# Kernel tuning notes

Hardware: AMD Instinct MI355X
Metric: run time of the kernel (lower is better)

The kernel has to match this reference:

```python
import jax, jax.numpy as jnp
import numpy as np
import math

B, T, D, H = 8, 1024, 512, 8
HD = D // H  # head_dim = 64


def setup_inputs() -> dict:
    key = jax.random.key(0)
    ks = jax.random.split(key, 16)
    s = 1.0 / math.sqrt(D)
    inp = {
        "x": jax.random.normal(ks[0], (B, T, D), jnp.float32),
        "pos": jax.random.normal(ks[1], (B, T, D), jnp.float32),
        "mask": jnp.ones((B, T, T), dtype=bool),
        "Wq": jax.random.normal(ks[2], (D, D), jnp.float32) * s,
        "bq": jax.random.normal(ks[3], (D,), jnp.float32) * s,
        "Wk": jax.random.normal(ks[4], (D, D), jnp.float32) * s,
        "bk": jax.random.normal(ks[5], (D,), jnp.float32) * s,
        "Wv": jax.random.normal(ks[6], (D, D), jnp.float32) * s,
        "bv": jax.random.normal(ks[7], (D,), jnp.float32) * s,
        "Wp": jax.random.normal(ks[8], (D, D), jnp.float32) * s,
        "Wo": jax.random.normal(ks[9], (D, D), jnp.float32) * s,
        "bo": jax.random.normal(ks[10], (D,), jnp.float32) * s,
        "pos_bias_u": jax.random.normal(ks[11], (H, HD), jnp.float32) * 0.02,
        "pos_bias_v": jax.random.normal(ks[12], (H, HD), jnp.float32) * 0.02,
    }
    return inp


def _shape(t):
    # [B, T, D] -> [B, H, T, HD]
    b, n, _ = t.shape
    return t.reshape(b, n, H, HD).transpose(0, 2, 1, 3)


def _relative_shift(s):
    # s: [B, H, Tq, Tk]
    b, h, tq, tk = s.shape
    s = jnp.pad(s, ((0, 0), (0, 0), (0, 0), (1, 0)))  # zero pad on left of last dim
    s = s.reshape(b, h, tk + 1, tq)[:, :, 1:, :].reshape(b, h, tq, tk)
    return s


def reference(x, pos, mask, Wq, bq, Wk, bk, Wv, bv, Wp, Wo, bo, pos_bias_u, pos_bias_v):
    q = _shape(x @ Wq + bq)          # [B,H,T,HD]
    k = _shape(x @ Wk + bk)
    v = _shape(x @ Wv + bv)
    p = _shape(pos @ Wp)             # pos_proj has no bias

    q_u = q + pos_bias_u[None, :, None, :]
    q_v = q + pos_bias_v[None, :, None, :]

    content = jnp.einsum("bhqd,bhkd->bhqk", q_u, k)
    position = jnp.einsum("bhqd,bhkd->bhqk", q_v, p)
    position = _relative_shift(position)[..., : content.shape[-1]]

    scores = (content + position) / math.sqrt(HD)
    scores = jnp.where(mask[:, None, :, :], scores, -1e9)
    attn = jax.nn.softmax(scores, axis=-1)

    ctx = jnp.einsum("bhqk,bhkd->bhqd", attn, v)
    ctx = ctx.transpose(0, 2, 1, 3).reshape(x.shape[0], x.shape[1], D)
    return ctx @ Wo + bo
```

## Files before the change

kernel.cpp:

```cpp
#include <hip/hip_runtime.h>
#include <cstdint>
#include <cstddef>

typedef unsigned short u16;
typedef unsigned int u32;
typedef __attribute__((ext_vector_type(8))) short bf16x8;
typedef __attribute__((ext_vector_type(4))) float f32x4;

#define LOG2E 1.4426950408889634f

__device__ __forceinline__ u16 f2bf(float f) {
  u32 u = __builtin_bit_cast(u32, f);
  u += 0x7fffu + ((u >> 16) & 1u);
  return (u16)(u >> 16);
}
__device__ __forceinline__ float bf2f(u16 h) {
  u32 u = ((u32)h) << 16;
  return __builtin_bit_cast(float, u);
}
__device__ __forceinline__ void g2l16(const void* g, void* l) {
  __builtin_amdgcn_global_load_lds((const __attribute__((address_space(1))) void*)g,
                                   (__attribute__((address_space(3))) void*)l, 16, 0, 0);
}

__global__ void cvt_bf16(const float* __restrict__ in, u16* __restrict__ out, int n) {
  int i = (blockIdx.x * blockDim.x + threadIdx.x) * 4;
  if (i >= n) return;
  float4 v = *(const float4*)(in + i);
  ushort4 o;
  o.x = f2bf(v.x); o.y = f2bf(v.y); o.z = f2bf(v.z); o.w = f2bf(v.w);
  *(ushort4*)(out + i) = o;
}

__global__ void transp_bf16(const float* __restrict__ W, u16* __restrict__ Wt) {
  __shared__ float t[64][65];
  const int n0 = blockIdx.x * 64, k0 = blockIdx.y * 64;
  const int tid = threadIdx.x;
  const int tx = tid & 63, ty = tid >> 6;
#pragma unroll
  for (int i = 0; i < 16; ++i) {
    int kl = ty + i * 4;
    t[kl][tx] = W[(size_t)(k0 + kl) * 512 + n0 + tx];
  }
  __syncthreads();
#pragma unroll
  for (int i = 0; i < 16; ++i) {
    int nl = ty + i * 4;
    Wt[(size_t)(n0 + nl) * 512 + k0 + tx] = f2bf(t[tx][nl]);
  }
}

__global__ __launch_bounds__(256, 2) void proj_gemm(
    const u16* __restrict__ xb, const u16* __restrict__ posb, const u16* __restrict__ Wt,
    const float* __restrict__ bq, const float* __restrict__ bk, const float* __restrict__ bv,
    const float* __restrict__ pbu, const float* __restrict__ pbv,
    u16* __restrict__ qu, u16* __restrict__ qv, u16* __restrict__ kb,
    u16* __restrict__ vT, u16* __restrict__ pb) {
  __shared__ __align__(16) u16 As[128 * 64];
  __shared__ __align__(16) u16 Bs[128 * 64];
  const int m0 = blockIdx.x * 128;
  const int nt = blockIdx.y;
  const int n0 = nt * 128;
  const int sec = nt >> 2;
  const u16* A = (sec == 3) ? posb : xb;
  const int tid = threadIdx.x;
  const int wid = tid >> 6, lane = tid & 63;
  const int wr = (wid >> 1) * 64, wc = (wid & 1) * 64;
  const int l15 = lane & 15, l4 = lane >> 4;
  f32x4 acc[4][4] = {};
  for (int k0 = 0; k0 < 512; k0 += 64) {
    __syncthreads();
#pragma unroll
    for (int i = 0; i < 4; ++i) {
      int s = tid + i * 256;
      int row = s >> 3, sl = s & 7, ssl = sl ^ (row & 7);
      g2l16(A + (size_t)(m0 + row) * 512 + k0 + ssl * 8, &As[s * 8]);
      g2l16(Wt + (size_t)(n0 + row) * 512 + k0 + ssl * 8, &Bs[s * 8]);
    }
    __syncthreads();
    bf16x8 af[4][2], bfr[4][2];
#pragma unroll
    for (int mi = 0; mi < 4; ++mi)
#pragma unroll
      for (int kk = 0; kk < 2; ++kk) {
        int row = wr + mi * 16 + l15;
        int slot = (kk * 4 + l4) ^ (row & 7);
        af[mi][kk] = *(const bf16x8*)&As[row * 64 + slot * 8];
      }
#pragma unroll
    for (int ni = 0; ni < 4; ++ni)
#pragma unroll
      for (int kk = 0; kk < 2; ++kk) {
        int row = wc + ni * 16 + l15;
        int slot = (kk * 4 + l4) ^ (row & 7);
        bfr[ni][kk] = *(const bf16x8*)&Bs[row * 64 + slot * 8];
      }
#pragma unroll
    for (int mi = 0; mi < 4; ++mi)
#pragma unroll
      for (int ni = 0; ni < 4; ++ni)
#pragma unroll
        for (int kk = 0; kk < 2; ++kk)
          acc[mi][ni] = __builtin_amdgcn_mfma_f32_16x16x32_bf16(af[mi][kk], bfr[ni][kk], acc[mi][ni], 0, 0, 0);
  }
#pragma unroll
  for (int mi = 0; mi < 4; ++mi)
#pragma unroll
    for (int ni = 0; ni < 4; ++ni) {
      int ng = n0 + wc + ni * 16 + l15;
      int cs = ng & 511;
      int h = cs >> 6, d = cs & 63;
      float bias = (sec == 0) ? bq[cs] : (sec == 1) ? bk[cs] : (sec == 2) ? bv[cs] : 0.f;
#pragma unroll
      for (int r = 0; r < 4; ++r) {
        int mg = m0 + wr + mi * 16 + l4 * 4 + r;
        int b = mg >> 10, t = mg & 1023;
        int bh = b * 8 + h;
        float val = acc[mi][ni][r] + bias;
        if (sec == 0) {
          size_t o = (size_t)bh * 65536 + (size_t)t * 64 + d;
          qu[o] = f2bf(val + pbu[cs]);
          qv[o] = f2bf(val + pbv[cs]);
        } else if (sec == 1) {
          kb[(size_t)bh * 65536 + (size_t)t * 64 + d] = f2bf(val);
        } else if (sec == 2) {
          vT[(size_t)bh * 65536 + (size_t)d * 1024 + t] = f2bf(val);
        } else {
          pb[(size_t)bh * 65536 + (size_t)t * 64 + d] = f2bf(val);
        }
      }
    }
}

__global__ __launch_bounds__(256, 2) void pos_shift_gemm(
    const u16* __restrict__ qv, const u16* __restrict__ pb, u16* __restrict__ spos) {
  __shared__ __align__(16) u16 As[128 * 64];
  __shared__ __align__(16) u16 Bs[128 * 64];
  const int bh = blockIdx.z;
  const int i0 = blockIdx.y * 128, j0 = blockIdx.x * 128;
  const u16* A = qv + (size_t)bh * 65536;
  const u16* B = pb + (size_t)bh * 65536;
  u16* S = spos + (size_t)bh * 1048576;
  const int tid = threadIdx.x;
  const int wid = tid >> 6, lane = tid & 63;
  const int wr = (wid >> 1) * 64, wc = (wid & 1) * 64;
  const int l15 = lane & 15, l4 = lane >> 4;
#pragma unroll
  for (int i = 0; i < 4; ++i) {
    int s = tid + i * 256;
    int row = s >> 3, sl = s & 7, ssl = sl ^ (row & 7);
    g2l16(A + (size_t)(i0 + row) * 64 + ssl * 8, &As[s * 8]);
    g2l16(B + (size_t)(j0 + row) * 64 + ssl * 8, &Bs[s * 8]);
  }
  __syncthreads();
  f32x4 acc[4][4] = {};
  bf16x8 af[4][2], bfr[4][2];
#pragma unroll
  for (int mi = 0; mi < 4; ++mi)
#pragma unroll
    for (int kk = 0; kk < 2; ++kk) {
      int row = wr + mi * 16 + l15;
      int slot = (kk * 4 + l4) ^ (row & 7);
      af[mi][kk] = *(const bf16x8*)&As[row * 64 + slot * 8];
    }
#pragma unroll
  for (int ni = 0; ni < 4; ++ni)
#pragma unroll
    for (int kk = 0; kk < 2; ++kk) {
      int row = wc + ni * 16 + l15;
      int slot = (kk * 4 + l4) ^ (row & 7);
      bfr[ni][kk] = *(const bf16x8*)&Bs[row * 64 + slot * 8];
    }
#pragma unroll
  for (int mi = 0; mi < 4; ++mi)
#pragma unroll
    for (int ni = 0; ni < 4; ++ni)
#pragma unroll
      for (int kk = 0; kk < 2; ++kk)
        acc[mi][ni] = __builtin_amdgcn_mfma_f32_16x16x32_bf16(af[mi][kk], bfr[ni][kk], acc[mi][ni], 0, 0, 0);
#pragma unroll
  for (int mi = 0; mi < 4; ++mi)
#pragma unroll
    for (int ni = 0; ni < 4; ++ni) {
      int j = j0 + wc + ni * 16 + l15;
#pragma unroll
      for (int r = 0; r < 4; ++r) {
        int i_ = i0 + wr + mi * 16 + l4 * 4 + r;
        float val = acc[mi][ni][r] * 0.125f;
        if (j >= 1023 - i_) {
          S[(size_t)i_ * 1024 + (size_t)(i_ + j - 1023)] = f2bf(val);
        } else if (i_ > 0) {
          S[(size_t)(i_ - 1) * 1024 + (size_t)(i_ + j + 1)] = f2bf(val);
        }
      }
    }
}

__global__ __launch_bounds__(256, 2) void flash_attn(
    const u16* __restrict__ qu, const u16* __restrict__ kb,
    const u16* __restrict__ vT, const u16* __restrict__ spos,
    u16* __restrict__ ctx) {
  __shared__ __align__(16) u16 Ks[64 * 64];
  __shared__ __align__(16) u16 Vs[64 * 64];
  __shared__ __align__(16) u16 Ss[64 * 64];
  __shared__ __align__(16) u16 Ps[4 * 16 * 64];
  const int q0 = blockIdx.x * 64;
  const int bh = blockIdx.y;
  const int b = bh >> 3, h = bh & 7;
  const int tid = threadIdx.x;
  const int w = tid >> 6, lane = tid & 63;
  const int l15 = lane & 15, l4 = lane >> 4;
  const u16* Q = qu + (size_t)bh * 65536;
  const u16* K = kb + (size_t)bh * 65536;
  const u16* V = vT + (size_t)bh * 65536;
  const u16* SP = spos + (size_t)bh * 1048576;
  bf16x8 aq[2];
#pragma unroll
  for (int kk = 0; kk < 2; ++kk)
    aq[kk] = *(const bf16x8*)(Q + (size_t)(q0 + w * 16 + l15) * 64 + kk * 32 + l4 * 8);
  f32x4 oacc[4] = {};
  float m_r[4], l_r[4];
#pragma unroll
  for (int r = 0; r < 4; ++r) { m_r[r] = -1e30f; l_r[r] = 0.f; }
  for (int kt = 0; kt < 16; ++kt) {
    const int k0 = kt * 64;
    __syncthreads();
#pragma unroll
    for (int i = 0; i < 2; ++i) {
      int s = tid + i * 256;
      int row = s >> 3, sl = s & 7, ssl = sl ^ (row & 7);
      g2l16(K + (size_t)(k0 + row) * 64 + ssl * 8, &Ks[s * 8]);
      g2l16(V + (size_t)row * 1024 + k0 + ssl * 8, &Vs[s * 8]);
      g2l16(SP + (size_t)(q0 + row) * 1024 + k0 + ssl * 8, &Ss[s * 8]);
    }
    __syncthreads();
    f32x4 sacc[4];
#pragma unroll
    for (int ni = 0; ni < 4; ++ni) {
      f32x4 a = {};
#pragma unroll
      for (int kk = 0; kk < 2; ++kk) {
        int key = ni * 16 + l15;
        int slot = (kk * 4 + l4) ^ (key & 7);
        bf16x8 bfr = *(const bf16x8*)&Ks[key * 64 + slot * 8];
        a = __builtin_amdgcn_mfma_f32_16x16x32_bf16(aq[kk], bfr, a, 0, 0, 0);
      }
      sacc[ni] = a;
    }
    float pvv[4][4], pmax[4];
#pragma unroll
    for (int r = 0; r < 4; ++r) pmax[r] = -1e30f;
#pragma unroll
    for (int ni = 0; ni < 4; ++ni)
#pragma unroll
      for (int r = 0; r < 4; ++r) {
        int srow = w * 16 + l4 * 4 + r;
        int scol = ni * 16 + l15;
        int slot = (scol >> 3) ^ (srow & 7);
        float sv = bf2f(Ss[srow * 64 + slot * 8 + (scol & 7)]);
        if (k0 + scol == q0 + srow + 1) sv = 0.f;
        float s_val = sacc[ni][r] * 0.125f + sv;
        pvv[ni][r] = s_val;
        pmax[r] = fmaxf(pmax[r], s_val);
      }
#pragma unroll
    for (int r = 0; r < 4; ++r)
#pragma unroll
      for (int off = 1; off < 16; off <<= 1)
        pmax[r] = fmaxf(pmax[r], __shfl_xor(pmax[r], off));
    float scl[4], rsum[4];
#pragma unroll
    for (int r = 0; r < 4; ++r) {
      float mn = fmaxf(m_r[r], pmax[r]);
      scl[r] = exp2f((m_r[r] - mn) * LOG2E);
      m_r[r] = mn;
      rsum[r] = 0.f;
    }
#pragma unroll
    for (int ni = 0; ni < 4; ++ni)
#pragma unroll
      for (int r = 0; r < 4; ++r) {
        float p = exp2f((pvv[ni][r] - m_r[r]) * LOG2E);
        pvv[ni][r] = p;
        rsum[r] += p;
      }
#pragma unroll
    for (int r = 0; r < 4; ++r) {
#pragma unroll
      for (int off = 1; off < 16; off <<= 1)
        rsum[r] += __shfl_xor(rsum[r], off);
      l_r[r] = l_r[r] * scl[r] + rsum[r];
    }
#pragma unroll
    for (int ni = 0; ni < 4; ++ni) {
      f32x4 o = oacc[ni];
      o[0] *= scl[0]; o[1] *= scl[1]; o[2] *= scl[2]; o[3] *= scl[3];
      oacc[ni] = o;
    }
#pragma unroll
    for (int ni = 0; ni < 4; ++ni)
#pragma unroll
      for (int r = 0; r < 4; ++r) {
        int prow = l4 * 4 + r;
        int col = ni * 16 + l15;
        int slot = (col >> 3) ^ (prow & 7);
        Ps[w * 1024 + prow * 64 + slot * 8 + (col & 7)] = f2bf(pvv[ni][r]);
      }
    bf16x8 pa[2];
#pragma unroll
    for (int kk = 0; kk < 2; ++kk) {
      int slot = (kk * 4 + l4) ^ (l15 & 7);
      pa[kk] = *(const bf16x8*)&Ps[w * 1024 + l15 * 64 + slot * 8];
    }
#pragma unroll
    for (int ni = 0; ni < 4; ++ni)
#pragma unroll
      for (int kk = 0; kk < 2; ++kk) {
        int drow = ni * 16 + l15;
        int slot = (kk * 4 + l4) ^ (drow & 7);
        bf16x8 vfr = *(const bf16x8*)&Vs[drow * 64 + slot * 8];
        oacc[ni] = __builtin_amdgcn_mfma_f32_16x16x32_bf16(pa[kk], vfr, oacc[ni], 0, 0, 0);
      }
  }
#pragma unroll
  for (int ni = 0; ni < 4; ++ni)
#pragma unroll
    for (int r = 0; r < 4; ++r) {
      int t = q0 + w * 16 + l4 * 4 + r;
      int d = ni * 16 + l15;
      ctx[((size_t)(b * 1024 + t)) * 512 + h * 64 + d] = f2bf(oacc[ni][r] / l_r[r]);
    }
}

__global__ __launch_bounds__(256, 2) void out_gemm(
    const u16* __restrict__ ctx, const u16* __restrict__ Wot,
    const float* __restrict__ bo, float* __restrict__ out) {
  __shared__ __align__(16) u16 As[128 * 64];
  __shared__ __align__(16) u16 Bs[128 * 64];
  const int m0 = blockIdx.x * 128;
  const int n0 = blockIdx.y * 128;
  const int tid = threadIdx.x;
  const int wid = tid >> 6, lane = tid & 63;
  const int wr = (wid >> 1) * 64, wc = (wid & 1) * 64;
  const int l15 = lane & 15, l4 = lane >> 4;
  f32x4 acc[4][4] = {};
  for (int k0 = 0; k0 < 512; k0 += 64) {
    __syncthreads();
#pragma unroll
    for (int i = 0; i < 4; ++i) {
      int s = tid + i * 256;
      int row = s >> 3, sl = s & 7, ssl = sl ^ (row & 7);
      g2l16(ctx + (size_t)(m0 + row) * 512 + k0 + ssl * 8, &As[s * 8]);
      g2l16(Wot + (size_t)(n0 + row) * 512 + k0 + ssl * 8, &Bs[s * 8]);
    }
    __syncthreads();
    bf16x8 af[4][2], bfr[4][2];
#pragma unroll
    for (int mi = 0; mi < 4; ++mi)
#pragma unroll
      for (int kk = 0; kk < 2; ++kk) {
        int row = wr + mi * 16 + l15;
        int slot = (kk * 4 + l4) ^ (row & 7);
        af[mi][kk] = *(const bf16x8*)&As[row * 64 + slot * 8];
      }
#pragma unroll
    for (int ni = 0; ni < 4; ++ni)
#pragma unroll
      for (int kk = 0; kk < 2; ++kk) {
        int row = wc + ni * 16 + l15;
        int slot = (kk * 4 + l4) ^ (row & 7);
        bfr[ni][kk] = *(const bf16x8*)&Bs[row * 64 + slot * 8];
      }
#pragma unroll
    for (int mi = 0; mi < 4; ++mi)
#pragma unroll
      for (int ni = 0; ni < 4; ++ni)
#pragma unroll
        for (int kk = 0; kk < 2; ++kk)
          acc[mi][ni] = __builtin_amdgcn_mfma_f32_16x16x32_bf16(af[mi][kk], bfr[ni][kk], acc[mi][ni], 0, 0, 0);
  }
#pragma unroll
  for (int mi = 0; mi < 4; ++mi)
#pragma unroll
    for (int ni = 0; ni < 4; ++ni) {
      int ng = n0 + wc + ni * 16 + l15;
      float bias = bo[ng];
#pragma unroll
      for (int r = 0; r < 4; ++r) {
        int mg = m0 + wr + mi * 16 + l4 * 4 + r;
        out[(size_t)mg * 512 + ng] = acc[mi][ni][r] + bias;
      }
    }
}

extern "C" void kernel_launch(void* const* d_in, const int* in_sizes, int n_in,
                              void* d_out, int out_size, void* d_ws, size_t ws_size,
                              hipStream_t stream) {
  const float* x   = (const float*)d_in[0];
  const float* pos = (const float*)d_in[1];
  const float* Wq  = (const float*)d_in[3];
  const float* bq  = (const float*)d_in[4];
  const float* Wk  = (const float*)d_in[5];
  const float* bk  = (const float*)d_in[6];
  const float* Wv  = (const float*)d_in[7];
  const float* bv  = (const float*)d_in[8];
  const float* Wp  = (const float*)d_in[9];
  const float* Wo  = (const float*)d_in[10];
  const float* bo  = (const float*)d_in[11];
  const float* pbu = (const float*)d_in[12];
  const float* pbv = (const float*)d_in[13];
  float* out = (float*)d_out;
  char* ws = (char*)d_ws;
  const size_t MB = 1024 * 1024;
  u16* x_bf   = (u16*)(ws);
  u16* pos_bf = (u16*)(ws + 8 * MB);
  u16* Wcat   = (u16*)(ws + 16 * MB);
  u16* Wot    = (u16*)(ws + 18 * MB);
  u16* qu     = (u16*)(ws + 19 * MB);
  u16* qv     = (u16*)(ws + 27 * MB);
  u16* kbuf   = (u16*)(ws + 35 * MB);
  u16* vbuf   = (u16*)(ws + 43 * MB);
  u16* pbuf   = (u16*)(ws + 51 * MB);
  u16* spos   = (u16*)(ws + 59 * MB);
  u16* ctxb   = (u16*)(ws + 187 * MB);

  cvt_bf16<<<4096, 256, 0, stream>>>(x, x_bf, 8192 * 512);
  cvt_bf16<<<4096, 256, 0, stream>>>(pos, pos_bf, 8192 * 512);
  dim3 tg(8, 8);
  transp_bf16<<<tg, 256, 0, stream>>>(Wq, Wcat);
  transp_bf16<<<tg, 256, 0, stream>>>(Wk, Wcat + 512 * 512);
  transp_bf16<<<tg, 256, 0, stream>>>(Wv, Wcat + 2 * 512 * 512);
  transp_bf16<<<tg, 256, 0, stream>>>(Wp, Wcat + 3 * 512 * 512);
  transp_bf16<<<tg, 256, 0, stream>>>(Wo, Wot);
  proj_gemm<<<dim3(64, 16), 256, 0, stream>>>(x_bf, pos_bf, Wcat, bq, bk, bv, pbu, pbv,
                                              qu, qv, kbuf, vbuf, pbuf);
  pos_shift_gemm<<<dim3(8, 8, 64), 256, 0, stream>>>(qv, pbuf, spos);
  flash_attn<<<dim3(16, 64), 256, 0, stream>>>(qu, kbuf, vbuf, spos, ctxb);
  out_gemm<<<dim3(64, 4), 256, 0, stream>>>(ctxb, Wot, bo, out);
}
```

Measured before the change: 326.9 us.

## Fuse relative-shift position scores into flash attention, drop materialized spos

Removes the separate pos_shift_gemm kernel that wrote a full B*H*T*T bf16 shifted position score tensor, and computes the position scores inside flash_attn per tile along diagonals (Q_v times a shifted range of P rows, plus one extra row for the wrap-around). K and V fragments are now read directly from global memory instead of being staged in LDS, and occupancy is raised to 3 blocks. This avoids roughly 128MB of write and read traffic, at the cost of extra MFMA work per tile (a 64x128 diagonal band plus a redundant wave-0 pass) and uncoalesced global fragment loads.

```diff
diff --git a/kernel.cpp b/kernel.cpp
--- a/kernel.cpp
+++ b/kernel.cpp
@@ -132,77 +132,11 @@
     }
 }
 
-__global__ __launch_bounds__(256, 2) void pos_shift_gemm(
-    const u16* __restrict__ qv, const u16* __restrict__ pb, u16* __restrict__ spos) {
-  __shared__ __align__(16) u16 As[128 * 64];
-  __shared__ __align__(16) u16 Bs[128 * 64];
-  const int bh = blockIdx.z;
-  const int i0 = blockIdx.y * 128, j0 = blockIdx.x * 128;
-  const u16* A = qv + (size_t)bh * 65536;
-  const u16* B = pb + (size_t)bh * 65536;
-  u16* S = spos + (size_t)bh * 1048576;
-  const int tid = threadIdx.x;
-  const int wid = tid >> 6, lane = tid & 63;
-  const int wr = (wid >> 1) * 64, wc = (wid & 1) * 64;
-  const int l15 = lane & 15, l4 = lane >> 4;
-#pragma unroll
-  for (int i = 0; i < 4; ++i) {
-    int s = tid + i * 256;
-    int row = s >> 3, sl = s & 7, ssl = sl ^ (row & 7);
-    g2l16(A + (size_t)(i0 + row) * 64 + ssl * 8, &As[s * 8]);
-    g2l16(B + (size_t)(j0 + row) * 64 + ssl * 8, &Bs[s * 8]);
-  }
-  __syncthreads();
-  f32x4 acc[4][4] = {};
-  bf16x8 af[4][2], bfr[4][2];
-#pragma unroll
-  for (int mi = 0; mi < 4; ++mi)
-#pragma unroll
-    for (int kk = 0; kk < 2; ++kk) {
-      int row = wr + mi * 16 + l15;
-      int slot = (kk * 4 + l4) ^ (row & 7);
-      af[mi][kk] = *(const bf16x8*)&As[row * 64 + slot * 8];
-    }
-#pragma unroll
-  for (int ni = 0; ni < 4; ++ni)
-#pragma unroll
-    for (int kk = 0; kk < 2; ++kk) {
-      int row = wc + ni * 16 + l15;
-      int slot = (kk * 4 + l4) ^ (row & 7);
-      bfr[ni][kk] = *(const bf16x8*)&Bs[row * 64 + slot * 8];
-    }
-#pragma unroll
-  for (int mi = 0; mi < 4; ++mi)
-#pragma unroll
-    for (int ni = 0; ni < 4; ++ni)
-#pragma unroll
-      for (int kk = 0; kk < 2; ++kk)
-        acc[mi][ni] = __builtin_amdgcn_mfma_f32_16x16x32_bf16(af[mi][kk], bfr[ni][kk], acc[mi][ni], 0, 0, 0);
-#pragma unroll
-  for (int mi = 0; mi < 4; ++mi)
-#pragma unroll
-    for (int ni = 0; ni < 4; ++ni) {
-      int j = j0 + wc + ni * 16 + l15;
-#pragma unroll
-      for (int r = 0; r < 4; ++r) {
-        int i_ = i0 + wr + mi * 16 + l4 * 4 + r;
-        float val = acc[mi][ni][r] * 0.125f;
-        if (j >= 1023 - i_) {
-          S[(size_t)i_ * 1024 + (size_t)(i_ + j - 1023)] = f2bf(val);
-        } else if (i_ > 0) {
-          S[(size_t)(i_ - 1) * 1024 + (size_t)(i_ + j + 1)] = f2bf(val);
-        }
-      }
-    }
-}
-
-__global__ __launch_bounds__(256, 2) void flash_attn(
-    const u16* __restrict__ qu, const u16* __restrict__ kb,
-    const u16* __restrict__ vT, const u16* __restrict__ spos,
-    u16* __restrict__ ctx) {
-  __shared__ __align__(16) u16 Ks[64 * 64];
-  __shared__ __align__(16) u16 Vs[64 * 64];
-  __shared__ __align__(16) u16 Ss[64 * 64];
+__global__ __launch_bounds__(256, 3) void flash_attn(
+    const u16* __restrict__ qu, const u16* __restrict__ qvg,
+    const u16* __restrict__ kb, const u16* __restrict__ vT,
+    const u16* __restrict__ pbuf, u16* __restrict__ ctx) {
+  __shared__ __align__(16) u16 Sqd[65 * 128];
   __shared__ __align__(16) u16 Ps[4 * 16 * 64];
   const int q0 = blockIdx.x * 64;
   const int bh = blockIdx.y;
@@ -211,27 +145,70 @@
   const int w = tid >> 6, lane = tid & 63;
   const int l15 = lane & 15, l4 = lane >> 4;
   const u16* Q = qu + (size_t)bh * 65536;
+  const u16* QV = qvg + (size_t)bh * 65536;
   const u16* K = kb + (size_t)bh * 65536;
   const u16* V = vT + (size_t)bh * 65536;
-  const u16* SP = spos + (size_t)bh * 1048576;
-  bf16x8 aq[2];
-#pragma unroll
-  for (int kk = 0; kk < 2; ++kk)
-    aq[kk] = *(const bf16x8*)(Q + (size_t)(q0 + w * 16 + l15) * 64 + kk * 32 + l4 * 8);
+  const u16* P = pbuf + (size_t)bh * 65536;
+  bf16x8 aq[2], aqv[2], aqv2[2];
+#pragma unroll
+  for (int kk = 0; kk < 2; ++kk) {
+    aq[kk]  = *(const bf16x8*)(Q  + (size_t)(q0 + w * 16 + l15) * 64 + kk * 32 + l4 * 8);
+    aqv[kk] = *(const bf16x8*)(QV + (size_t)(q0 + w * 16 + l15) * 64 + kk * 32 + l4 * 8);
+  }
+  {
+    int r2 = min(q0 + 64 + l15, 1023);
+#pragma unroll
+    for (int kk = 0; kk < 2; ++kk)
+      aqv2[kk] = *(const bf16x8*)(QV + (size_t)r2 * 64 + kk * 32 + l4 * 8);
+  }
   f32x4 oacc[4] = {};
   float m_r[4], l_r[4];
 #pragma unroll
   for (int r = 0; r < 4; ++r) { m_r[r] = -1e30f; l_r[r] = 0.f; }
   for (int kt = 0; kt < 16; ++kt) {
     const int k0 = kt * 64;
-    __syncthreads();
-#pragma unroll
-    for (int i = 0; i < 2; ++i) {
-      int s = tid + i * 256;
-      int row = s >> 3, sl = s & 7, ssl = sl ^ (row & 7);
-      g2l16(K + (size_t)(k0 + row) * 64 + ssl * 8, &Ks[s * 8]);
-      g2l16(V + (size_t)row * 1024 + k0 + ssl * 8, &Vs[s * 8]);
-      g2l16(SP + (size_t)(q0 + row) * 1024 + k0 + ssl * 8, &Ss[s * 8]);
+    const int dbase = k0 - q0 - 63;
+    __syncthreads();
+#pragma unroll
+    for (int half = 0; half < 2; ++half) {
+      f32x4 pacc[4] = {};
+#pragma unroll
+      for (int ni = 0; ni < 4; ++ni)
+#pragma unroll
+        for (int kk = 0; kk < 2; ++kk) {
+          int n = half * 64 + ni * 16 + l15;
+          int d = dbase + n;
+          int jp = (d <= 0) ? (1023 + d) : (d - 2);
+          jp = min(max(jp, 0), 1023);
+          bf16x8 bp = *(const bf16x8*)(P + (size_t)jp * 64 + kk * 32 + l4 * 8);
+          pacc[ni] = __builtin_amdgcn_mfma_f32_16x16x32_bf16(aqv[kk], bp, pacc[ni], 0, 0, 0);
+        }
+#pragma unroll
+      for (int ni = 0; ni < 4; ++ni)
+#pragma unroll
+        for (int r = 0; r < 4; ++r)
+          Sqd[(w * 16 + l4 * 4 + r) * 128 + half * 64 + ni * 16 + l15] = f2bf(pacc[ni][r] * 0.125f);
+    }
+    if (w == 0) {
+#pragma unroll
+      for (int half = 0; half < 2; ++half) {
+        f32x4 pacc[4] = {};
+#pragma unroll
+        for (int ni = 0; ni < 4; ++ni)
+#pragma unroll
+          for (int kk = 0; kk < 2; ++kk) {
+            int n = half * 64 + ni * 16 + l15;
+            int d = dbase + n;
+            int jp = (d <= 0) ? (1023 + d) : (d - 2);
+            jp = min(max(jp, 0), 1023);
+            bf16x8 bp = *(const bf16x8*)(P + (size_t)jp * 64 + kk * 32 + l4 * 8);
+            pacc[ni] = __builtin_amdgcn_mfma_f32_16x16x32_bf16(aqv2[kk], bp, pacc[ni], 0, 0, 0);
+          }
+        if (l4 == 0)
+#pragma unroll
+          for (int ni = 0; ni < 4; ++ni)
+            Sqd[64 * 128 + half * 64 + ni * 16 + l15] = f2bf(pacc[ni][0] * 0.125f);
+      }
     }
     __syncthreads();
     f32x4 sacc[4];
@@ -240,10 +217,8 @@
       f32x4 a = {};
 #pragma unroll
       for (int kk = 0; kk < 2; ++kk) {
-        int key = ni * 16 + l15;
-        int slot = (kk * 4 + l4) ^ (key & 7);
-        bf16x8 bfr = *(const bf16x8*)&Ks[key * 64 + slot * 8];
-        a = __builtin_amdgcn_mfma_f32_16x16x32_bf16(aq[kk], bfr, a, 0, 0, 0);
+        bf16x8 bk_ = *(const bf16x8*)(K + (size_t)(k0 + ni * 16 + l15) * 64 + kk * 32 + l4 * 8);
+        a = __builtin_amdgcn_mfma_f32_16x16x32_bf16(aq[kk], bk_, a, 0, 0, 0);
       }
       sacc[ni] = a;
     }
@@ -256,9 +231,9 @@
       for (int r = 0; r < 4; ++r) {
         int srow = w * 16 + l4 * 4 + r;
         int scol = ni * 16 + l15;
-        int slot = (scol >> 3) ^ (srow & 7);
-        float sv = bf2f(Ss[srow * 64 + slot * 8 + (scol & 7)]);
-        if (k0 + scol == q0 + srow + 1) sv = 0.f;
+        int D = k0 + scol - q0 - srow;
+        float sv = (D == 1) ? 0.f
+                            : bf2f(Sqd[(srow + (D >= 2)) * 128 + 63 + scol - srow]);
         float s_val = sacc[ni][r] * 0.125f + sv;
         pvv[ni][r] = s_val;
         pmax[r] = fmaxf(pmax[r], s_val);
@@ -316,9 +291,7 @@
     for (int ni = 0; ni < 4; ++ni)
 #pragma unroll
       for (int kk = 0; kk < 2; ++kk) {
-        int drow = ni * 16 + l15;
-        int slot = (kk * 4 + l4) ^ (drow & 7);
-        bf16x8 vfr = *(const bf16x8*)&Vs[drow * 64 + slot * 8];
+        bf16x8 vfr = *(const bf16x8*)(V + (size_t)(ni * 16 + l15) * 1024 + k0 + kk * 32 + l4 * 8);
         oacc[ni] = __builtin_amdgcn_mfma_f32_16x16x32_bf16(pa[kk], vfr, oacc[ni], 0, 0, 0);
       }
   }
@@ -421,8 +394,7 @@
   u16* kbuf   = (u16*)(ws + 35 * MB);
   u16* vbuf   = (u16*)(ws + 43 * MB);
   u16* pbuf   = (u16*)(ws + 51 * MB);
-  u16* spos   = (u16*)(ws + 59 * MB);
-  u16* ctxb   = (u16*)(ws + 187 * MB);
+  u16* ctxb   = (u16*)(ws + 59 * MB);
 
   cvt_bf16<<<4096, 256, 0, stream>>>(x, x_bf, 8192 * 512);
   cvt_bf16<<<4096, 256, 0, stream>>>(pos, pos_bf, 8192 * 512);
@@ -434,7 +406,6 @@
   transp_bf16<<<tg, 256, 0, stream>>>(Wo, Wot);
   proj_gemm<<<dim3(64, 16), 256, 0, stream>>>(x_bf, pos_bf, Wcat, bq, bk, bv, pbu, pbv,
                                               qu, qv, kbuf, vbuf, pbuf);
-  pos_shift_gemm<<<dim3(8, 8, 64), 256, 0, stream>>>(qv, pbuf, spos);
-  flash_attn<<<dim3(16, 64), 256, 0, stream>>>(qu, kbuf, vbuf, spos, ctxb);
+  flash_attn<<<dim3(16, 64), 256, 0, stream>>>(qu, qv, kbuf, vbuf, pbuf, ctxb);
   out_gemm<<<dim3(64, 4), 256, 0, stream>>>(ctxb, Wot, bo, out);
 }
```

New measurement: 571.6 us. +74.9%, slower.
